# Kernel tuning notes

Measured on AMD Instinct MI355X. Metric: run time of the kernel, lower is better.

## Reference

```python
import jax, jax.numpy as jnp
import numpy as np

N = 100_000      # nodes
E = 1_600_000    # edges (avg degree 16)
IN, H, OUT = 960, 192, 3
NB = 6           # block_num


def setup_inputs() -> dict:
    key = jax.random.key(0)
    ks = jax.random.split(key, 14)
    s = 0.05  # weight init scale
    x = jax.random.normal(ks[0], (N, IN), jnp.float32)
    src = jax.random.randint(ks[1], (E,), 0, N, jnp.int32)
    dst = jax.random.randint(ks[2], (E,), 0, N, jnp.int32)
    # normalized adjacency values (like D^-1 A entries)
    ew = jax.random.uniform(ks[3], (E,), jnp.float32) / 16.0
    w1 = jax.random.normal(ks[4], (IN, H), jnp.float32) * s
    l1 = jax.random.normal(ks[5], (IN, H), jnp.float32) * s
    b1 = jnp.zeros((H,), jnp.float32)
    wb = jax.random.normal(ks[6], (2 * NB, H, H), jnp.float32) * s
    lb = jax.random.normal(ks[7], (2 * NB, H, H), jnp.float32) * s
    bb = jnp.zeros((2 * NB, H), jnp.float32)
    w2 = jax.random.normal(ks[8], (H, OUT), jnp.float32) * s
    l2 = jax.random.normal(ks[9], (H, OUT), jnp.float32) * s
    b2 = jnp.zeros((OUT,), jnp.float32)
    return dict(x=x, src=src, dst=dst, ew=ew, w1=w1, l1=l1, b1=b1,
                wb=wb, lb=lb, bb=bb, w2=w2, l2=l2, b2=b2)


def reference(x, src, dst, ew, w1, l1, b1, wb, lb, bb, w2, l2, b2):
    def gcn(h, w, lw, b):
        # GraphConvolution: spmm(adj, h @ w) + h @ loop_w + b
        sup = h @ w                                   # [N, F_out]
        msg = sup[src] * ew[:, None]                  # gather + weight  [E, F_out]
        agg = jax.ops.segment_sum(msg, dst, num_segments=N)
        return agg + h @ lw + b

    h = gcn(x, w1, l1, b1)                            # conv1: in_dim -> hidden
    for i in range(NB):                               # GResBlocks
        a = gcn(h, wb[2 * i], lb[2 * i], bb[2 * i])
        a = gcn(a, wb[2 * i + 1], lb[2 * i + 1], bb[2 * i + 1])
        h = (h + a) * 0.5                             # residual scaling
    x_cat = h
    x_out = gcn(x_cat, w2, l2, b2)                    # conv2: hidden -> out_dim
    return (x_out, x_cat)
```

## Files before the change

### kernel.cpp

```cpp
#include <hip/hip_runtime.h>

typedef __attribute__((ext_vector_type(8))) short short8;
typedef __attribute__((ext_vector_type(4))) float f32x4;
typedef __attribute__((ext_vector_type(4))) int int4v;
typedef __attribute__((ext_vector_type(2))) unsigned int u32x2;

__device__ __forceinline__ float bf2f(unsigned short u) {
  return __uint_as_float(((unsigned)u) << 16);
}
__device__ __forceinline__ unsigned short f2bf(float f) {
  unsigned u = __float_as_uint(f);
  return (unsigned short)((u + 0x7FFFu + ((u >> 16) & 1u)) >> 16);
}

#define GLB_CAST(p) ((const __attribute__((address_space(1))) void*)(p))
#define LDS_CAST(p) ((__attribute__((address_space(3))) void*)(p))

__global__ void count_kernel(const int* __restrict__ dst, int* __restrict__ cnt, int E) {
  int e = blockIdx.x * blockDim.x + threadIdx.x;
  if (e < E) atomicAdd(&cnt[dst[e] + 1], 1);
}

__global__ __launch_bounds__(256) void scan_bsum_kernel(const int* __restrict__ cnt,
                                                        int* __restrict__ bsum, int n) {
  __shared__ int buf[256];
  int tid = threadIdx.x;
  int j0 = blockIdx.x * 1024 + tid * 4;
  int s = 0;
#pragma unroll
  for (int k = 0; k < 4; k++) {
    int j = j0 + k;
    if (j < n) s += cnt[j];
  }
  buf[tid] = s;
  __syncthreads();
  for (int off = 128; off > 0; off >>= 1) {
    if (tid < off) buf[tid] += buf[tid + off];
    __syncthreads();
  }
  if (tid == 0) bsum[blockIdx.x] = buf[0];
}

__global__ __launch_bounds__(256) void scan_small_kernel(const int* __restrict__ bsum,
                                                         int* __restrict__ boff, int nb) {
  __shared__ int buf[2][256];
  int tid = threadIdx.x;
  int C = (nb + 255) >> 8;
  int start = tid * C;
  int end = start + C; if (end > nb) end = nb;
  int s = 0;
  for (int j = start; j < end; j++) s += bsum[j];
  buf[0][tid] = s;
  __syncthreads();
  int pin = 0;
  for (int off = 1; off < 256; off <<= 1) {
    int v = buf[pin][tid];
    if (tid >= off) v += buf[pin][tid - off];
    buf[pin ^ 1][tid] = v;
    pin ^= 1;
    __syncthreads();
  }
  int run = (tid == 0) ? 0 : buf[pin][tid - 1];
  for (int j = start; j < end; j++) {
    boff[j] = run;
    run += bsum[j];
  }
}

__global__ __launch_bounds__(256) void scan_final_kernel(const int* __restrict__ cnt,
                                                         const int* __restrict__ boff,
                                                         int* __restrict__ rowptr,
                                                         int* __restrict__ cur,
                                                         int n, int nrows) {
  __shared__ int buf[2][256];
  int tid = threadIdx.x;
  int j0 = blockIdx.x * 1024 + tid * 4;
  int v[4];
  int s = 0;
#pragma unroll
  for (int k = 0; k < 4; k++) {
    int j = j0 + k;
    v[k] = (j < n) ? cnt[j] : 0;
    s += v[k];
  }
  buf[0][tid] = s;
  __syncthreads();
  int pin = 0;
  for (int off = 1; off < 256; off <<= 1) {
    int t = buf[pin][tid];
    if (tid >= off) t += buf[pin][tid - off];
    buf[pin ^ 1][tid] = t;
    pin ^= 1;
    __syncthreads();
  }
  int run = boff[blockIdx.x] + ((tid == 0) ? 0 : buf[pin][tid - 1]);
#pragma unroll
  for (int k = 0; k < 4; k++) {
    int j = j0 + k;
    if (j < n) {
      run += v[k];
      rowptr[j] = run;
      if (j < nrows) cur[j] = run;
    }
  }
}

__global__ void fill_kernel(const int* __restrict__ src, const int* __restrict__ dst,
                            const float* __restrict__ ew,
                            int* __restrict__ cur, int2* __restrict__ s_edge, int E) {
  int e = blockIdx.x * blockDim.x + threadIdx.x;
  if (e >= E) return;
  int r = dst[e];
  int pos = atomicAdd(&cur[r], 1);
  s_edge[pos] = make_int2(src[e], __float_as_int(ew[e]));
}

__global__ void prep_w_kernel(const float* __restrict__ w1,
                              const float* __restrict__ l1,
                              const float* __restrict__ wb,
                              const float* __restrict__ lb,
                              unsigned short* __restrict__ Wt1,
                              unsigned short* __restrict__ Wcatb) {
  int tid = blockIdx.x * blockDim.x + threadIdx.x;
  const int n1 = 384 * 960;
  const int nc = 12 * 192 * 384;
  if (tid < n1) {
    int c = tid / 960, k = tid % 960;
    Wt1[tid] = f2bf((c < 192) ? w1[k * 192 + c] : l1[k * 192 + (c - 192)]);
  } else if (tid < n1 + nc) {
    int u = tid - n1;
    int i = u / (192 * 384);
    int r = u % (192 * 384);
    int c = r / 384, k = r % 384;
    Wcatb[u] = f2bf((k < 192) ? wb[((size_t)i * 192 + k) * 192 + c]
                              : lb[((size_t)i * 192 + (k - 192)) * 192 + c]);
  }
}

__device__ __forceinline__ short8 cvt_pair(f32x4 a, f32x4 b) {
  short8 r;
  r[0] = (short)f2bf(a[0]); r[1] = (short)f2bf(a[1]);
  r[2] = (short)f2bf(a[2]); r[3] = (short)f2bf(a[3]);
  r[4] = (short)f2bf(b[0]); r[5] = (short)f2bf(b[1]);
  r[6] = (short)f2bf(b[2]); r[7] = (short)f2bf(b[3]);
  return r;
}

__global__ __launch_bounds__(512) void gemm_f32_kernel(const float* __restrict__ A,
                                                       const unsigned short* __restrict__ Wt,
                                                       unsigned short* __restrict__ out,
                                                       int nrows, int K) {
  __shared__ char lds_raw[40960];

  int tid = threadIdx.x;
  int lane = tid & 63;
  int w = tid >> 6;
  int rg = w >> 1, ch = w & 1;
  int row0blk = blockIdx.x * 256;
  int row0 = row0blk + rg * 64;
  int l15 = lane & 15, lq = lane >> 4;

  f32x4 acc[12][4];
#pragma unroll
  for (int cf = 0; cf < 12; cf++)
#pragma unroll
    for (int rf = 0; rf < 4; rf++) acc[cf][rf] = (f32x4)(0.0f);

  int tiles = K / 32;
  for (int tile = 0; tile < tiles; ++tile) {
    __syncthreads();
#pragma unroll
    for (int it = 0; it < 3; ++it) {
      int slot = it * 512 + tid;
      int q = slot / 384, c = slot - q * 384;
      const unsigned short* g = Wt + (size_t)c * K + tile * 32 + q * 8;
      __builtin_amdgcn_global_load_lds(GLB_CAST(g), LDS_CAST(lds_raw + 16384 + slot * 16), 16, 0, 0);
    }
#pragma unroll
    for (int it = 0; it < 2; ++it) {
      int slot = it * 512 + tid;
      int c = slot >> 8, row = slot & 255;
      int grow = row0blk + row;
      if (grow > nrows - 1) grow = nrows - 1;
      const float* g = A + (size_t)grow * K + tile * 32 + c * 8;
      f32x4 a0 = *reinterpret_cast<const f32x4*>(g);
      f32x4 a1 = *reinterpret_cast<const f32x4*>(g + 4);
      *reinterpret_cast<short8*>(lds_raw + slot * 16) = cvt_pair(a0, a1);
    }
    __syncthreads();

    short8 af[4];
#pragma unroll
    for (int rf = 0; rf < 4; rf++)
      af[rf] = *reinterpret_cast<const short8*>(
          lds_raw + lq * 4096 + (rg * 64 + rf * 16 + l15) * 16);
#pragma unroll
    for (int cf = 0; cf < 12; cf++) {
      const short8 bf = *reinterpret_cast<const short8*>(
          lds_raw + 16384 + (lq * 384 + ch * 192 + cf * 16 + l15) * 16);
#pragma unroll
      for (int rf = 0; rf < 4; rf++)
        acc[cf][rf] = __builtin_amdgcn_mfma_f32_16x16x32_bf16(bf, af[rf], acc[cf][rf], 0, 0, 0);
    }
  }

#pragma unroll
  for (int rf = 0; rf < 4; rf++) {
    int row = row0 + rf * 16 + l15;
    if (row >= nrows) continue;
    unsigned short* orow = out + (size_t)row * 384 + ch * 192 + lq * 4;
#pragma unroll
    for (int cf = 0; cf < 12; cf++) {
      u32x2 pv;
      pv[0] = (unsigned)f2bf(acc[cf][rf][0]) | ((unsigned)f2bf(acc[cf][rf][1]) << 16);
      pv[1] = (unsigned)f2bf(acc[cf][rf][2]) | ((unsigned)f2bf(acc[cf][rf][3]) << 16);
      *reinterpret_cast<u32x2*>(orow + cf * 16) = pv;
    }
  }
}

__global__ __launch_bounds__(256) void spmm_t_kernel(const unsigned short* __restrict__ t,
                                                     const int* __restrict__ rowptr,
                                                     const int2* __restrict__ s_edge,
                                                     const float* __restrict__ bias,
                                                     unsigned short* __restrict__ out16,
                                                     int n) {
  int tid = blockIdx.x * blockDim.x + threadIdx.x;
  int node = tid >> 3;
  int sub = tid & 7;
  if (node >= n) return;
  int co = sub * 8;

  float acc[3][8];
#pragma unroll
  for (int q = 0; q < 3; q++)
#pragma unroll
    for (int j = 0; j < 8; j++) acc[q][j] = 0.0f;

  int e0 = rowptr[node], e1 = rowptr[node + 1];
  int ne = e1 - e0;
  int base = 0;
  for (; base + 8 <= ne; base += 8) {
    int2 rec = s_edge[e0 + base + sub];
#pragma unroll
    for (int half = 0; half < 2; half++) {
      short8 v[4][3];
      float wgt[4];
#pragma unroll
      for (int k = 0; k < 4; k++) {
        int kk = half * 4 + k;
        int sn = __shfl(rec.x, kk, 8);
        wgt[k] = __int_as_float(__shfl(rec.y, kk, 8));
        const unsigned short* row = t + (size_t)sn * 384;
#pragma unroll
        for (int q = 0; q < 3; q++)
          v[k][q] = *reinterpret_cast<const short8*>(row + q * 64 + co);
      }
#pragma unroll
      for (int k = 0; k < 4; k++)
#pragma unroll
        for (int q = 0; q < 3; q++)
#pragma unroll
          for (int j = 0; j < 8; j++)
            acc[q][j] += wgt[k] * bf2f((unsigned short)v[k][q][j]);
    }
  }
  for (; base < ne; base++) {
    int2 rec = s_edge[e0 + base];
    float wgt = __int_as_float(rec.y);
    const unsigned short* row = t + (size_t)rec.x * 384;
#pragma unroll
    for (int q = 0; q < 3; q++) {
      short8 v = *reinterpret_cast<const short8*>(row + q * 64 + co);
#pragma unroll
      for (int j = 0; j < 8; j++) acc[q][j] += wgt * bf2f((unsigned short)v[j]);
    }
  }

  const unsigned short* hlrow = t + (size_t)node * 384 + 192;
#pragma unroll
  for (int q = 0; q < 3; q++) {
    short8 hlv = *reinterpret_cast<const short8*>(hlrow + q * 64 + co);
    unsigned short o16[8];
#pragma unroll
    for (int j = 0; j < 8; j++)
      o16[j] = f2bf(acc[q][j] + bf2f((unsigned short)hlv[j]) + bias[q * 64 + co + j]);
    *reinterpret_cast<int4v*>(&out16[(size_t)node * 192 + q * 64 + co]) =
        *reinterpret_cast<const int4v*>(o16);
  }
}

__global__ __launch_bounds__(512) void fused_res_kernel(const unsigned short* __restrict__ h,
                                                        const int* __restrict__ rowptr,
                                                        const int2* __restrict__ s_edge,
                                                        const unsigned short* __restrict__ Wcat,
                                                        const float* __restrict__ bias,
                                                        const unsigned short* __restrict__ hprev,
                                                        unsigned short* __restrict__ outp,
                                                        int n) {
  extern __shared__ char lds[];
  const int BOFF = 49152;

  int tid = threadIdx.x;
  int lane = tid & 63;
  int row0 = blockIdx.x * 128;

  {
    int nloc = tid >> 2;
    int sub = tid & 3;
    int grow = row0 + nloc;
    if (grow > n - 1) grow = n - 1;
    float acc[6][8];
#pragma unroll
    for (int jq = 0; jq < 6; jq++)
#pragma unroll
      for (int j = 0; j < 8; j++) acc[jq][j] = 0.0f;

    int e0 = rowptr[grow], e1 = rowptr[grow + 1];
    int ne = e1 - e0;
    int base = 0;
    for (; base + 4 <= ne; base += 4) {
      int2 rec = s_edge[e0 + base + sub];
#pragma unroll
      for (int kp = 0; kp < 2; kp++) {
        short8 v[2][6];
        float wg[2];
#pragma unroll
        for (int k = 0; k < 2; k++) {
          int kk = kp * 2 + k;
          int sn = __shfl(rec.x, kk, 4);
          wg[k] = __int_as_float(__shfl(rec.y, kk, 4));
          const unsigned short* rowp = h + (size_t)sn * 192;
#pragma unroll
          for (int jq = 0; jq < 6; jq++)
            v[k][jq] = *reinterpret_cast<const short8*>(rowp + (jq * 4 + sub) * 8);
        }
#pragma unroll
        for (int k = 0; k < 2; k++)
#pragma unroll
          for (int jq = 0; jq < 6; jq++)
#pragma unroll
            for (int j = 0; j < 8; j++)
              acc[jq][j] += wg[k] * bf2f((unsigned short)v[k][jq][j]);
      }
    }
    for (; base < ne; base++) {
      int2 rec = s_edge[e0 + base];
      float wg = __int_as_float(rec.y);
      const unsigned short* rowp = h + (size_t)rec.x * 192;
#pragma unroll
      for (int jq = 0; jq < 6; jq++) {
        short8 v = *reinterpret_cast<const short8*>(rowp + (jq * 4 + sub) * 8);
#pragma unroll
        for (int j = 0; j < 8; j++) acc[jq][j] += wg * bf2f((unsigned short)v[j]);
      }
    }
#pragma unroll
    for (int jq = 0; jq < 6; jq++) {
      int q = jq * 4 + sub;
      unsigned short o[8];
#pragma unroll
      for (int j = 0; j < 8; j++) o[j] = f2bf(acc[jq][j]);
      *reinterpret_cast<int4v*>(lds + (q * 128 + nloc) * 16) =
          *reinterpret_cast<const int4v*>(o);
    }
  }

  auto stageB = [&](int t, int buf) {
    {
      int slot = tid;
      int q = slot / 192, c = slot - q * 192;
      const unsigned short* g = Wcat + (size_t)c * 384 + t * 32 + q * 8;
      __builtin_amdgcn_global_load_lds(GLB_CAST(g),
                                       LDS_CAST(lds + BOFF + buf * 12288 + slot * 16), 16, 0, 0);
    }
    if (tid < 256) {
      int slot = 512 + tid;
      int q = slot / 192, c = slot - q * 192;
      const unsigned short* g = Wcat + (size_t)c * 384 + t * 32 + q * 8;
      __builtin_amdgcn_global_load_lds(GLB_CAST(g),
                                       LDS_CAST(lds + BOFF + buf * 12288 + slot * 16), 16, 0, 0);
    }
  };

  stageB(0, 0);
  __syncthreads();

  int rg = tid >> 6;
  int l15 = lane & 15, lq = lane >> 4;
  f32x4 acc[12];
#pragma unroll
  for (int cf = 0; cf < 12; cf++) acc[cf] = (f32x4)(0.0f);

  for (int t = 0; t < 12; ++t) {
    if (t + 1 < 12) {
      stageB(t + 1, (t + 1) & 1);
      if (t + 1 >= 6) {
        int slot = tid;
        int q = slot >> 7, row = slot & 127;
        int grow = row0 + row;
        if (grow > n - 1) grow = n - 1;
        const unsigned short* g = h + (size_t)grow * 192 + (t + 1 - 6) * 32 + q * 8;
        __builtin_amdgcn_global_load_lds(GLB_CAST(g),
                                         LDS_CAST(lds + ((t + 1) & 1) * 8192 + slot * 16), 16, 0, 0);
      }
    }

    short8 af;
    if (t < 6)
      af = *reinterpret_cast<const short8*>(lds + ((t * 4 + lq) * 128 + rg * 16 + l15) * 16);
    else
      af = *reinterpret_cast<const short8*>(lds + (t & 1) * 8192 + (lq * 128 + rg * 16 + l15) * 16);

#pragma unroll
    for (int cf = 0; cf < 12; cf++) {
      const short8 bf = *reinterpret_cast<const short8*>(
          lds + BOFF + (t & 1) * 12288 + (lq * 192 + cf * 16 + l15) * 16);
      acc[cf] = __builtin_amdgcn_mfma_f32_16x16x32_bf16(bf, af, acc[cf], 0, 0, 0);
    }
    __syncthreads();
  }

  int row = row0 + rg * 16 + l15;
  if (row < n) {
    unsigned short* orow = outp + (size_t)row * 192 + lq * 4;
#pragma unroll
    for (int cf = 0; cf < 12; cf++) {
      int col = cf * 16 + lq * 4;
      f32x4 bv = *reinterpret_cast<const f32x4*>(bias + col);
      float r[4];
#pragma unroll
      for (int j = 0; j < 4; j++) r[j] = acc[cf][j] + bv[j];
      if (hprev) {
        u32x2 hp = *reinterpret_cast<const u32x2*>(&hprev[(size_t)row * 192 + col]);
        r[0] = 0.5f * (bf2f((unsigned short)(hp[0] & 0xFFFF)) + r[0]);
        r[1] = 0.5f * (bf2f((unsigned short)(hp[0] >> 16)) + r[1]);
        r[2] = 0.5f * (bf2f((unsigned short)(hp[1] & 0xFFFF)) + r[2]);
        r[3] = 0.5f * (bf2f((unsigned short)(hp[1] >> 16)) + r[3]);
      }
      u32x2 pv;
      pv[0] = (unsigned)f2bf(r[0]) | ((unsigned)f2bf(r[1]) << 16);
      pv[1] = (unsigned)f2bf(r[2]) | ((unsigned)f2bf(r[3]) << 16);
      *reinterpret_cast<u32x2*>(orow + cf * 16) = pv;
    }
  }
}

__global__ __launch_bounds__(256) void cvt_kernel(const unsigned short* __restrict__ h16,
                                                  float* __restrict__ h32, int n8) {
  int i = blockIdx.x * blockDim.x + threadIdx.x;
  if (i >= n8) return;
  short8 v = *reinterpret_cast<const short8*>(&h16[(size_t)i * 8]);
  f32x4 lo, hi;
#pragma unroll
  for (int j = 0; j < 4; j++) {
    lo[j] = bf2f((unsigned short)v[j]);
    hi[j] = bf2f((unsigned short)v[4 + j]);
  }
  *reinterpret_cast<f32x4*>(&h32[(size_t)i * 8]) = lo;
  *reinterpret_cast<f32x4*>(&h32[(size_t)i * 8 + 4]) = hi;
}

__global__ __launch_bounds__(256) void conv2a_kernel(const unsigned short* __restrict__ h,
                                                     const float* __restrict__ w2,
                                                     const float* __restrict__ l2,
                                                     const float* __restrict__ b2,
                                                     float* __restrict__ sup2,
                                                     float* __restrict__ hl2, int n) {
  int wid = (blockIdx.x * blockDim.x + threadIdx.x) >> 6;
  int lane = threadIdx.x & 63;
  if (wid >= n) return;
  float sa[3] = {0.f, 0.f, 0.f}, sl[3] = {0.f, 0.f, 0.f};
  for (int k = lane; k < 192; k += 64) {
    float hv = bf2f(h[(size_t)wid * 192 + k]);
#pragma unroll
    for (int j = 0; j < 3; j++) {
      sa[j] += hv * w2[k * 3 + j];
      sl[j] += hv * l2[k * 3 + j];
    }
  }
#pragma unroll
  for (int j = 0; j < 3; j++) {
    for (int off = 32; off > 0; off >>= 1) {
      sa[j] += __shfl_down(sa[j], off);
      sl[j] += __shfl_down(sl[j], off);
    }
  }
  if (lane == 0) {
#pragma unroll
    for (int j = 0; j < 3; j++) {
      sup2[(size_t)wid * 3 + j] = sa[j];
      hl2[(size_t)wid * 3 + j] = sl[j] + b2[j];
    }
  }
}

__global__ __launch_bounds__(256) void conv2b_kernel(const int* __restrict__ rowptr,
                                                     const int2* __restrict__ s_edge,
                                                     const float* __restrict__ sup2,
                                                     const float* __restrict__ hl2,
                                                     float* __restrict__ out, int n) {
  int node = blockIdx.x * blockDim.x + threadIdx.x;
  if (node >= n) return;
  float acc[3] = {0.f, 0.f, 0.f};
  int e0 = rowptr[node], e1 = rowptr[node + 1];
  for (int e = e0; e < e1; e++) {
    int2 rec = s_edge[e];
    float wgt = __int_as_float(rec.y);
#pragma unroll
    for (int j = 0; j < 3; j++) acc[j] += wgt * sup2[(size_t)rec.x * 3 + j];
  }
#pragma unroll
  for (int j = 0; j < 3; j++)
    out[(size_t)node * 3 + j] = acc[j] + hl2[(size_t)node * 3 + j];
}

extern "C" void kernel_launch(void* const* d_in, const int* in_sizes, int n_in,
                              void* d_out, int out_size, void* d_ws, size_t ws_size,
                              hipStream_t stream) {
  const float* x  = (const float*)d_in[0];
  const int* src  = (const int*)d_in[1];
  const int* dst  = (const int*)d_in[2];
  const float* ew = (const float*)d_in[3];
  const float* w1 = (const float*)d_in[4];
  const float* l1 = (const float*)d_in[5];
  const float* b1 = (const float*)d_in[6];
  const float* wb = (const float*)d_in[7];
  const float* lb = (const float*)d_in[8];
  const float* bb = (const float*)d_in[9];
  const float* w2 = (const float*)d_in[10];
  const float* l2 = (const float*)d_in[11];
  const float* b2 = (const float*)d_in[12];
  float* out = (float*)d_out;

  const int N = in_sizes[0] / 960;
  const int E = in_sizes[1];

  float* h32 = out + (size_t)N * 3;

  char* p = (char*)d_ws;
  auto alloc = [&](size_t bytes) {
    char* q = p;
    p += (bytes + 255) & ~(size_t)255;
    return q;
  };
  unsigned short* Wt1   = (unsigned short*)alloc((size_t)384 * 960 * 2);
  unsigned short* Wcatb = (unsigned short*)alloc((size_t)12 * 192 * 384 * 2);
  unsigned short* t     = (unsigned short*)alloc((size_t)N * 384 * 2);
  unsigned short* h16a  = (unsigned short*)alloc((size_t)N * 192 * 2);
  unsigned short* h16b  = (unsigned short*)alloc((size_t)N * 192 * 2);
  int* rowptr = (int*)alloc((size_t)(N + 1) * 4);
  int* cur    = (int*)alloc((size_t)N * 4);
  int* cnt    = (int*)alloc((size_t)(N + 1) * 4);
  int* bsum   = (int*)alloc((size_t)1024 * 4);
  int* boff   = (int*)alloc((size_t)1024 * 4);
  int2* s_edge = (int2*)alloc((size_t)E * 8);
  float* sup2 = (float*)alloc((size_t)N * 3 * 4);
  float* hl2  = (float*)alloc((size_t)N * 3 * 4);
  if ((size_t)(p - (char*)d_ws) > ws_size) return;

  unsigned short* a16 = t;

  const int nScan = N + 1;
  const int nBlk = (nScan + 1023) / 1024;

  hipMemsetAsync(cnt, 0, (size_t)(N + 1) * 4, stream);
  count_kernel<<<(E + 255) / 256, 256, 0, stream>>>(dst, cnt, E);
  scan_bsum_kernel<<<nBlk, 256, 0, stream>>>(cnt, bsum, nScan);
  scan_small_kernel<<<1, 256, 0, stream>>>(bsum, boff, nBlk);
  scan_final_kernel<<<nBlk, 256, 0, stream>>>(cnt, boff, rowptr, cur, nScan, N);
  fill_kernel<<<(E + 255) / 256, 256, 0, stream>>>(src, dst, ew, cur, s_edge, E);
  {
    int total = 384 * 960 + 12 * 192 * 384;
    prep_w_kernel<<<(total + 255) / 256, 256, 0, stream>>>(w1, l1, wb, lb, Wt1, Wcatb);
  }

  int gBlocks = (N + 255) / 256;
  int sBlocks = (N * 8 + 255) / 256;
  int fBlocks = (N + 127) / 128;
  const int F_LDS = 73728;

  gemm_f32_kernel<<<gBlocks, 512, 0, stream>>>(x, Wt1, t, N, 960);
  spmm_t_kernel<<<sBlocks, 256, 0, stream>>>(t, rowptr, s_edge, b1, h16a, N);

  unsigned short* hcur = h16a;
  unsigned short* hnxt = h16b;
  for (int i = 0; i < 12; i += 2) {
    fused_res_kernel<<<fBlocks, 512, F_LDS, stream>>>(
        hcur, rowptr, s_edge, Wcatb + (size_t)i * 192 * 384, bb + (size_t)i * 192,
        (const unsigned short*)nullptr, a16, N);
    fused_res_kernel<<<fBlocks, 512, F_LDS, stream>>>(
        a16, rowptr, s_edge, Wcatb + (size_t)(i + 1) * 192 * 384, bb + (size_t)(i + 1) * 192,
        hcur, hnxt, N);
    unsigned short* tmp = hcur; hcur = hnxt; hnxt = tmp;
  }

  cvt_kernel<<<(N * 24 + 255) / 256, 256, 0, stream>>>(hcur, h32, N * 24);

  conv2a_kernel<<<(N + 3) / 4, 256, 0, stream>>>(hcur, w2, l2, b2, sup2, hl2, N);
  conv2b_kernel<<<(N + 255) / 256, 256, 0, stream>>>(rowptr, s_edge, sup2, hl2, out, N);
}
```

Measured before the change: 2.501 ms.

## Halve fused residual block tile to 64 rows and keep self-loop A fragments in registers

The fused aggregation+GEMM kernel now processes 64 rows per 256-thread block instead of 128 rows per 512 threads, shrinking LDS from 72KB to 48KB and allowing three blocks per CU via launch bounds. The self-loop half of the A operand (the node's own features) is loaded directly into registers up front rather than staged through double-buffered LDS, removing those async copies. The aim is more resident blocks and less LDS traffic, at the cost of more register pressure and reloading the weight tile twice as often per row.

Result: faster. 2.419 ms (-3.3%).

```diff
diff --git a/kernel.cpp b/kernel.cpp
--- a/kernel.cpp
+++ b/kernel.cpp
@@ -290,20 +290,29 @@
   }
 }
 
-__global__ __launch_bounds__(512) void fused_res_kernel(const unsigned short* __restrict__ h,
-                                                        const int* __restrict__ rowptr,
-                                                        const int2* __restrict__ s_edge,
-                                                        const unsigned short* __restrict__ Wcat,
-                                                        const float* __restrict__ bias,
-                                                        const unsigned short* __restrict__ hprev,
-                                                        unsigned short* __restrict__ outp,
-                                                        int n) {
+__global__ __launch_bounds__(256, 3) void fused_res_kernel(const unsigned short* __restrict__ h,
+                                                           const int* __restrict__ rowptr,
+                                                           const int2* __restrict__ s_edge,
+                                                           const unsigned short* __restrict__ Wcat,
+                                                           const float* __restrict__ bias,
+                                                           const unsigned short* __restrict__ hprev,
+                                                           unsigned short* __restrict__ outp,
+                                                           int n) {
   extern __shared__ char lds[];
-  const int BOFF = 49152;
+  const int BOFF = 24576;
 
   int tid = threadIdx.x;
   int lane = tid & 63;
-  int row0 = blockIdx.x * 128;
+  int row0 = blockIdx.x * 64;
+  int rg = tid >> 6;
+  int l15 = lane & 15, lq = lane >> 4;
+
+  int myrow = row0 + rg * 16 + l15;
+  int myrowc = myrow > n - 1 ? n - 1 : myrow;
+  short8 hfrag[6];
+#pragma unroll
+  for (int t = 0; t < 6; t++)
+    hfrag[t] = *reinterpret_cast<const short8*>(h + (size_t)myrowc * 192 + t * 32 + lq * 8);
 
   {
     int nloc = tid >> 2;
@@ -361,56 +370,37 @@
       unsigned short o[8];
 #pragma unroll
       for (int j = 0; j < 8; j++) o[j] = f2bf(acc[jq][j]);
-      *reinterpret_cast<int4v*>(lds + (q * 128 + nloc) * 16) =
+      *reinterpret_cast<int4v*>(lds + (q * 64 + nloc) * 16) =
           *reinterpret_cast<const int4v*>(o);
     }
   }
 
   auto stageB = [&](int t, int buf) {
-    {
-      int slot = tid;
+#pragma unroll
+    for (int it = 0; it < 3; ++it) {
+      int slot = it * 256 + tid;
       int q = slot / 192, c = slot - q * 192;
       const unsigned short* g = Wcat + (size_t)c * 384 + t * 32 + q * 8;
       __builtin_amdgcn_global_load_lds(GLB_CAST(g),
                                        LDS_CAST(lds + BOFF + buf * 12288 + slot * 16), 16, 0, 0);
     }
-    if (tid < 256) {
-      int slot = 512 + tid;
-      int q = slot / 192, c = slot - q * 192;
-      const unsigned short* g = Wcat + (size_t)c * 384 + t * 32 + q * 8;
-      __builtin_amdgcn_global_load_lds(GLB_CAST(g),
-                                       LDS_CAST(lds + BOFF + buf * 12288 + slot * 16), 16, 0, 0);
-    }
   };
 
   stageB(0, 0);
   __syncthreads();
 
-  int rg = tid >> 6;
-  int l15 = lane & 15, lq = lane >> 4;
   f32x4 acc[12];
 #pragma unroll
   for (int cf = 0; cf < 12; cf++) acc[cf] = (f32x4)(0.0f);
 
   for (int t = 0; t < 12; ++t) {
-    if (t + 1 < 12) {
-      stageB(t + 1, (t + 1) & 1);
-      if (t + 1 >= 6) {
-        int slot = tid;
-        int q = slot >> 7, row = slot & 127;
-        int grow = row0 + row;
-        if (grow > n - 1) grow = n - 1;
-        const unsigned short* g = h + (size_t)grow * 192 + (t + 1 - 6) * 32 + q * 8;
-        __builtin_amdgcn_global_load_lds(GLB_CAST(g),
-                                         LDS_CAST(lds + ((t + 1) & 1) * 8192 + slot * 16), 16, 0, 0);
-      }
-    }
+    if (t + 1 < 12) stageB(t + 1, (t + 1) & 1);
 
     short8 af;
     if (t < 6)
-      af = *reinterpret_cast<const short8*>(lds + ((t * 4 + lq) * 128 + rg * 16 + l15) * 16);
+      af = *reinterpret_cast<const short8*>(lds + ((t * 4 + lq) * 64 + rg * 16 + l15) * 16);
     else
-      af = *reinterpret_cast<const short8*>(lds + (t & 1) * 8192 + (lq * 128 + rg * 16 + l15) * 16);
+      af = hfrag[t - 6];
 
 #pragma unroll
     for (int cf = 0; cf < 12; cf++) {
@@ -421,9 +411,8 @@
     __syncthreads();
   }
 
-  int row = row0 + rg * 16 + l15;
-  if (row < n) {
-    unsigned short* orow = outp + (size_t)row * 192 + lq * 4;
+  if (myrow < n) {
+    unsigned short* orow = outp + (size_t)myrow * 192 + lq * 4;
 #pragma unroll
     for (int cf = 0; cf < 12; cf++) {
       int col = cf * 16 + lq * 4;
@@ -432,7 +421,7 @@
 #pragma unroll
       for (int j = 0; j < 4; j++) r[j] = acc[cf][j] + bv[j];
       if (hprev) {
-        u32x2 hp = *reinterpret_cast<const u32x2*>(&hprev[(size_t)row * 192 + col]);
+        u32x2 hp = *reinterpret_cast<const u32x2*>(&hprev[(size_t)myrow * 192 + col]);
         r[0] = 0.5f * (bf2f((unsigned short)(hp[0] & 0xFFFF)) + r[0]);
         r[1] = 0.5f * (bf2f((unsigned short)(hp[0] >> 16)) + r[1]);
         r[2] = 0.5f * (bf2f((unsigned short)(hp[1] & 0xFFFF)) + r[2]);
@@ -577,8 +566,8 @@
 
   int gBlocks = (N + 255) / 256;
   int sBlocks = (N * 8 + 255) / 256;
-  int fBlocks = (N + 127) / 128;
-  const int F_LDS = 73728;
+  int fBlocks = (N + 63) / 64;
+  const int F_LDS = 49152;
 
   gemm_f32_kernel<<<gBlocks, 512, 0, stream>>>(x, Wt1, t, N, 960);
   spmm_t_kernel<<<sBlocks, 256, 0, stream>>>(t, rowptr, s_edge, b1, h16a, N);
@@ -586,10 +575,10 @@
   unsigned short* hcur = h16a;
   unsigned short* hnxt = h16b;
   for (int i = 0; i < 12; i += 2) {
-    fused_res_kernel<<<fBlocks, 512, F_LDS, stream>>>(
+    fused_res_kernel<<<fBlocks, 256, F_LDS, stream>>>(
         hcur, rowptr, s_edge, Wcatb + (size_t)i * 192 * 384, bb + (size_t)i * 192,
         (const unsigned short*)nullptr, a16, N);
-    fused_res_kernel<<<fBlocks, 512, F_LDS, stream>>>(
+    fused_res_kernel<<<fBlocks, 256, F_LDS, stream>>>(
         a16, rowptr, s_edge, Wcatb + (size_t)(i + 1) * 192 * 384, bb + (size_t)(i + 1) * 192,
         hcur, hnxt, N);
     unsigned short* tmp = hcur; hcur = hnxt; hnxt = tmp;
```
